# Optimization experiments

Hardware: AMD Instinct MI355X
Metric: run time of the kernel (lower is better)

Reference implementation:

```python
import jax, jax.numpy as jnp
import numpy as np

T, B, C = 512, 4, 256   # seq, batch, in_features
R = 256                 # reduce_dim (== in_features == out_features, required by original view/matmul)
OUT = 256
NE = 64                 # n experts / codebook size
D = R * OUT             # 65536, centroid dimension
TAU = 1.0               # gumbel temperature
DECAY = 0.999           # EMA decay
COMMIT = 0.25           # commitment scale


def setup_inputs() -> dict:
    key = jax.random.key(0)
    ks = jax.random.split(key, 6)
    x = jax.random.normal(ks[0], (T, B, C), dtype=jnp.float32)
    # uniform noise for gumbel sampling (kept as input for determinism)
    u_noise = jax.random.uniform(ks[1], (T * B, NE), dtype=jnp.float32,
                                 minval=1e-6, maxval=1.0 - 1e-6)
    W_map = jax.random.normal(ks[2], (D, C), dtype=jnp.float32) * 0.02   # xavier-ish
    b_map = jnp.zeros((D,), jnp.float32)
    pw_w1 = jax.random.normal(ks[3], (1, 1, R, C), dtype=jnp.float32) * (1.0 / np.sqrt(R))
    pw_B = jnp.zeros((1, 1, OUT), jnp.float32)   # 'constant' bias mode, init 0
    centroids = jax.random.normal(ks[4], (NE, D), dtype=jnp.float32) * 0.5  # init_centroids std
    return {"x": x, "u_noise": u_noise, "W_map": W_map, "b_map": b_map,
            "pw_w1": pw_w1, "pw_B": pw_B, "centroids": centroids}


def reference(x, u_noise, W_map, b_map, pw_w1, pw_B, centroids):
    N = T * B
    # key projection: [N, D]
    keyf = x.reshape(N, C) @ W_map.T + b_map
    kd = jax.lax.stop_gradient(keyf)  # assign() uses points.data

    # squared euclidean cdist: ||p||^2 + ||c||^2 - 2 p c^T   [N, NE]
    d2 = (kd * kd).sum(1, keepdims=True) \
         + (centroids * centroids).sum(1)[None, :] \
         - 2.0 * (kd @ centroids.T)

    # gumbel-softmax routing (soft, hard=False); resp detached (depends only on data)
    g = -jnp.log(-jnp.log(u_noise))
    resp = jax.nn.softmax((-d2 + g) / TAU, axis=-1)  # [N, NE]

    # vectorized EMA centroid update (original loops over experts; math identical,
    # mean_assigned[i] = mean_n resp[n,i]*key[n] = (resp^T @ key)/N), detached in original
    mean_assigned = (resp.T @ kd) / N                # [NE, D]
    centroids_new = DECAY * centroids + (1.0 - DECAY) * mean_assigned

    # quantized U-vectors from UPDATED centroids (update precedes matmul in original)
    quantized = resp @ centroids_new                 # [N, D]

    # euclid commitment loss (quantized detached)
    loss = COMMIT * jnp.mean((keyf - jax.lax.stop_gradient(quantized)) ** 2)

    # dynamic per-token weight: w = quantized.view(T,B,R,C) @ pw_w1  -> [T,B,R,C]
    w2 = jnp.einsum('tbik,kj->tbij', quantized.reshape(T, B, R, C), pw_w1[0, 0])
    # apply to input: [T,B,R,C] @ [T,B,C] -> [T,B,OUT]  (R == OUT)
    out = jnp.einsum('tbij,tbj->tbi', w2, x) + pw_B  # constant bias broadcasts
    return (out, loss)
```

## Files before the change

### kernel.cpp

```cpp
#include <hip/hip_runtime.h>
#include <hip/hip_bf16.h>

constexpr int N_TOK = 2048;
constexpr int C_    = 256;
constexpr int NE    = 64;
constexpr int D_    = 65536;
constexpr float DECAYF = 0.999f;
constexpr float OMD    = 0.001f;
constexpr float ALPHA  = OMD / 2048.0f;
constexpr float RTHRESH = 1e-5f;
constexpr int CHMAX = 8448;

using bf16x8 = __attribute__((ext_vector_type(8))) short;
using f32x4  = __attribute__((ext_vector_type(4))) float;
using u16 = unsigned short;

constexpr size_t OFF_XSUM  = 65536;
constexpr size_t OFF_G     = 65792;
constexpr size_t OFF_M     = 131328;
constexpr size_t OFF_WB    = 147712;
constexpr size_t OFF_BB    = 147968;
constexpr size_t OFF_SUMR  = 147984;
constexpr size_t OFF_A     = 148048;
constexpr size_t OFF_CC0   = 164432;
constexpr size_t OFF_RR    = 168528;
constexpr size_t OFF_CNT   = 172624;
constexpr size_t OFF_CB    = 172752;
constexpr size_t OFF_TSLOT = 172816;
constexpr size_t ZFLOATS   = 174864;
constexpr size_t OFF_RESP  = 174864;
constexpr size_t OFF_AG    = 174864;
constexpr size_t OFF_MA    = 191248;
constexpr size_t OFF_AGA   = 195344;
constexpr size_t OFF_AWB   = 199440;
constexpr size_t OFF_CHE   = 199504;
constexpr size_t OFF_CHB   = 207952;
constexpr size_t OFF_NCH   = 216400;
constexpr size_t OFF_Y     = 305936;
constexpr size_t OFF_CNEW  = 830224;
constexpr size_t OFF_TIDX  = 5024528;
constexpr size_t OFF_TOKR  = 5155600;
constexpr size_t OFF_WTH   = 5286672;
constexpr size_t OFF_SCG   = 13675280;
constexpr size_t OFF_SCC   = 16296720;
constexpr size_t WS_FAST2_END = 18393872;

__device__ __forceinline__ unsigned pack_bf2(float a, float b) {
  __hip_bfloat16 ha = __float2bfloat16(a), hb = __float2bfloat16(b);
  unsigned short ua = *reinterpret_cast<unsigned short*>(&ha);
  unsigned short ub = *reinterpret_cast<unsigned short*>(&hb);
  return (unsigned)ua | ((unsigned)ub << 16);
}

__global__ __launch_bounds__(256) void k_preTw(const float* __restrict__ bmap,
    const float* __restrict__ x, const float* __restrict__ W,
    float* __restrict__ bb, float* __restrict__ xsum, float* __restrict__ Wb,
    u16* __restrict__ wth) {
  __shared__ __align__(16) char smem[32896];
  int bx = blockIdx.x;
  int t = threadIdx.x;
  if (bx < 4) {
    float* red = (float*)smem;
    int base = bx * 16384 + t;
    float s = 0.f;
    for (int q = 0; q < 64; q++) { float v = bmap[base + q * 256]; s = fmaf(v, v, s); }
    red[t] = s;
    __syncthreads();
    for (int k = 128; k > 0; k >>= 1) {
      if (t < k) red[t] += red[t + k];
      __syncthreads();
    }
    if (t == 0) atomicAdd(&bb[0], red[0]);
  } else if (bx < 36) {
    int n0 = (bx - 4) * 64;
    float s = 0.f;
    for (int n = 0; n < 64; n++) s += x[(n0 + n) * C_ + t];
    atomicAdd(&xsum[t], s);
  } else if (bx < 292) {
    float* bs = (float*)smem;
    __shared__ int any;
    int d0 = (bx - 36) * 256;
    if (t == 0) any = 0;
    __syncthreads();
    float bv = bmap[d0 + t];
    bs[t] = bv;
    if (bv != 0.f) any = 1;
    __syncthreads();
    if (any == 0) return;
    float s = 0.f;
    for (int d = 0; d < 256; d++) s = fmaf(bs[d], W[(size_t)(d0 + d) * C_ + t], s);
    atomicAdd(&Wb[t], s);
  } else {
    float (*Ls)[257] = (float(*)[257])smem;
    int d0 = (bx - 292) * 32;
    int r = t >> 3, c8 = (t & 7) * 32;
    #pragma unroll
    for (int q = 0; q < 8; q++) {
      float4 v = *(const float4*)&W[(size_t)(d0 + r) * 256 + c8 + q * 4];
      Ls[r][c8 + q * 4 + 0] = v.x; Ls[r][c8 + q * 4 + 1] = v.y;
      Ls[r][c8 + q * 4 + 2] = v.z; Ls[r][c8 + q * 4 + 3] = v.w;
    }
    __syncthreads();
    int dq = (t & 3) * 8;
    #pragma unroll
    for (int pQ = 0; pQ < 4; pQ++) {
      int c = pQ * 64 + (t >> 2);
      unsigned hw[4];
      #pragma unroll
      for (int q = 0; q < 4; q++)
        hw[q] = pack_bf2(Ls[dq + 2 * q][c], Ls[dq + 2 * q + 1][c]);
      size_t o = (size_t)c * 65536 + d0 + dq;
      *(uint4*)&wth[o] = make_uint4(hw[0], hw[1], hw[2], hw[3]);
    }
  }
}

__global__ __launch_bounds__(256) void k_big1(const u16* __restrict__ wth,
    const float* __restrict__ cen, const float* __restrict__ W,
    const float* __restrict__ bmap, float* __restrict__ gpart,
    float* __restrict__ mpart, float* __restrict__ cpart, float* __restrict__ cb) {
  __shared__ __align__(16) char smem[17408];
  int bx = blockIdx.x;
  int t = threadIdx.x;
  if (bx < 640) {
    u16* Ta = (u16*)smem;
    u16* Tb = Ta + 4352;
    int kb = bx & 63, p = bx >> 6;
    int ti = 0, rem0 = p;
    while (rem0 >= 4 - ti) { rem0 -= 4 - ti; ti++; }
    int tj = ti + rem0;
    bool two = (ti != tj);
    const u16* srcA = wth + (size_t)(ti * 64) * 65536;
    const u16* srcB = wth + (size_t)(tj * 64) * 65536;
    int l = t & 63, w = t >> 6;
    int m0 = w * 16, lm = l & 15, g = l >> 4;
    int scol = t >> 3, skseg = t & 7;
    f32x4 acc[4] = {};
    for (int cc = 0; cc < 16; cc++) {
      int k0 = kb * 1024 + cc * 64;
      __syncthreads();
      {
        uint4 a0 = *(const uint4*)(srcA + (size_t)scol * 65536 + k0 + skseg * 8);
        uint4 a1 = *(const uint4*)(srcA + (size_t)(scol + 32) * 65536 + k0 + skseg * 8);
        *(uint4*)(Ta + (skseg * 68 + scol) * 8) = a0;
        *(uint4*)(Ta + (skseg * 68 + scol + 32) * 8) = a1;
        if (two) {
          uint4 b0 = *(const uint4*)(srcB + (size_t)scol * 65536 + k0 + skseg * 8);
          uint4 b1 = *(const uint4*)(srcB + (size_t)(scol + 32) * 65536 + k0 + skseg * 8);
          *(uint4*)(Tb + (skseg * 68 + scol) * 8) = b0;
          *(uint4*)(Tb + (skseg * 68 + scol + 32) * 8) = b1;
        }
      }
      __syncthreads();
      const u16* TBp = two ? Tb : Ta;
      #pragma unroll
      for (int ks = 0; ks < 2; ks++) {
        int kq = ks * 4 + g;
        bf16x8 av = *(const bf16x8*)(Ta + (kq * 68 + m0 + lm) * 8);
        #pragma unroll
        for (int j = 0; j < 4; j++) {
          bf16x8 bv = *(const bf16x8*)(TBp + (kq * 68 + j * 16 + lm) * 8);
          acc[j] = __builtin_amdgcn_mfma_f32_16x16x32_bf16(av, bv, acc[j], 0, 0, 0);
        }
      }
    }
    float* pp = &gpart[((size_t)p * 64 + kb) * 4096];
    #pragma unroll
    for (int j = 0; j < 4; j++)
      #pragma unroll
      for (int r = 0; r < 4; r++)
        pp[(m0 + (l >> 4) * 4 + r) * 64 + j * 16 + lm] = acc[j][r];
  } else if (bx < 1664) {
    float (*As)[68] = (float(*)[68])smem;
    float (*Bs)[68] = (float(*)[68])(smem + 8704);
    int idx = bx - 640;
    int kb = idx & 255, c0 = (idx >> 8) * 64;
    int d0 = kb * 256;
    int tx = t & 15, ty = t >> 4;
    int e = t >> 2, dg = t & 3;
    int lr = t >> 3, lc = (t & 7) * 8;
    float acc[4][4] = {};
    for (int dk = 0; dk < 256; dk += 32) {
      const float* cr = &cen[(size_t)e * D_ + d0 + dk];
      float4 cv0 = *(const float4*)&cr[dg * 4];
      float4 cv1 = *(const float4*)&cr[16 + dg * 4];
      const float* wr = &W[(size_t)(d0 + dk + lr) * C_ + c0];
      float4 w0 = *(const float4*)&wr[lc];
      float4 w1 = *(const float4*)&wr[lc + 4];
      __syncthreads();
      As[dg * 4 + 0][e] = cv0.x; As[dg * 4 + 1][e] = cv0.y;
      As[dg * 4 + 2][e] = cv0.z; As[dg * 4 + 3][e] = cv0.w;
      As[16 + dg * 4 + 0][e] = cv1.x; As[16 + dg * 4 + 1][e] = cv1.y;
      As[16 + dg * 4 + 2][e] = cv1.z; As[16 + dg * 4 + 3][e] = cv1.w;
      *(float4*)&Bs[lr][lc]     = w0;
      *(float4*)&Bs[lr][lc + 4] = w1;
      __syncthreads();
      #pragma unroll 8
      for (int k = 0; k < 32; k++) {
        float4 ra4 = *(const float4*)&As[k][ty * 4];
        float4 rb4 = *(const float4*)&Bs[k][tx * 4];
        float ra[4] = {ra4.x, ra4.y, ra4.z, ra4.w};
        float rb[4] = {rb4.x, rb4.y, rb4.z, rb4.w};
        #pragma unroll
        for (int i = 0; i < 4; i++)
          #pragma unroll
          for (int j = 0; j < 4; j++)
            acc[i][j] = fmaf(ra[i], rb[j], acc[i][j]);
      }
    }
    float* pp = &mpart[(size_t)kb * 16384];
    #pragma unroll
    for (int i = 0; i < 4; i++)
      *(float4*)&pp[(ty * 4 + i) * C_ + c0 + tx * 4] = *(float4*)&acc[i][0];
  } else {
    float (*cs)[68] = (float(*)[68])smem;
    float* red = (float*)(smem + 8704);
    int d0 = (bx - 1664) * 128;
    int e = t >> 2, dg = t & 3;
    int tx = t & 15, ty = t >> 4;
    float acc[4][4] = {};
    float cbp = 0.f;
    for (int dk = 0; dk < 128; dk += 32) {
      const float* cr = &cen[(size_t)e * D_ + d0 + dk];
      float4 v0 = *(const float4*)&cr[dg * 4];
      float4 v1 = *(const float4*)&cr[16 + dg * 4];
      const float* br = &bmap[d0 + dk];
      float4 b0 = *(const float4*)&br[dg * 4];
      float4 b1 = *(const float4*)&br[16 + dg * 4];
      cbp += v0.x * b0.x + v0.y * b0.y + v0.z * b0.z + v0.w * b0.w
           + v1.x * b1.x + v1.y * b1.y + v1.z * b1.z + v1.w * b1.w;
      __syncthreads();
      cs[dg * 4 + 0][e] = v0.x; cs[dg * 4 + 1][e] = v0.y;
      cs[dg * 4 + 2][e] = v0.z; cs[dg * 4 + 3][e] = v0.w;
      cs[16 + dg * 4 + 0][e] = v1.x; cs[16 + dg * 4 + 1][e] = v1.y;
      cs[16 + dg * 4 + 2][e] = v1.z; cs[16 + dg * 4 + 3][e] = v1.w;
      __syncthreads();
      #pragma unroll
      for (int k = 0; k < 32; k++) {
        float4 ra4 = *(const float4*)&cs[k][ty * 4];
        float4 rb4 = *(const float4*)&cs[k][tx * 4];
        float ra[4] = {ra4.x, ra4.y, ra4.z, ra4.w};
        float rb[4] = {rb4.x, rb4.y, rb4.z, rb4.w};
        #pragma unroll
        for (int i = 0; i < 4; i++)
          #pragma unroll
          for (int j = 0; j < 4; j++)
            acc[i][j] = fmaf(ra[i], rb[j], acc[i][j]);
      }
    }
    float* pp = &cpart[(size_t)(bx - 1664) * 4096];
    #pragma unroll
    for (int i = 0; i < 4; i++)
      *(float4*)&pp[(ty * 4 + i) * 64 + tx * 4] = *(float4*)&acc[i][0];
    red[t] = cbp;
    __syncthreads();
    if (t < 64)
      atomicAdd(&cb[t], red[t * 4] + red[t * 4 + 1] + red[t * 4 + 2] + red[t * 4 + 3]);
  }
}

__global__ __launch_bounds__(256) void k_redAll(const float* __restrict__ gp,
    const float* __restrict__ mp, const float* __restrict__ cp,
    float* __restrict__ G, float* __restrict__ M, float* __restrict__ CC0) {
  int bx = blockIdx.x;
  if (bx < 160) {
    int p = bx / 16, ib = bx % 16;
    int ti = 0, rem0 = p;
    while (rem0 >= 4 - ti) { rem0 -= 4 - ti; ti++; }
    int tj = ti + rem0;
    int i = ib * 256 + threadIdx.x;
    const float* base = gp + (size_t)p * 64 * 4096 + i;
    float s = 0.f;
    for (int kb = 0; kb < 64; kb++) s += base[(size_t)kb * 4096];
    int r = i >> 6, c = i & 63;
    G[(ti * 64 + r) * C_ + tj * 64 + c] = s;
    if (ti != tj) G[(tj * 64 + c) * C_ + ti * 64 + r] = s;
  } else if (bx < 416) {
    int idx = bx - 160;
    int i = (idx & 63) * 256 + threadIdx.x;
    int kb0 = (idx >> 6) * 64;
    float s = 0.f;
    #pragma unroll 8
    for (int kb = 0; kb < 64; kb++) s += mp[(size_t)(kb0 + kb) * 16384 + i];
    atomicAdd(&M[i], s);
  } else {
    int idx = bx - 416;
    int i = (idx & 15) * 256 + threadIdx.x;
    int kb0 = (idx >> 4) * 64;
    float s = 0.f;
    #pragma unroll 8
    for (int kb = 0; kb < 64; kb++) s += cp[(size_t)(kb0 + kb) * 4096 + i];
    atomicAdd(&CC0[i], s);
  }
}

__global__ __launch_bounds__(256) void k_big2(const float* __restrict__ x,
    const float* __restrict__ pw, const float* __restrict__ G,
    const float* __restrict__ u, const float* __restrict__ M,
    const float* __restrict__ CC0, const float* __restrict__ cb,
    float* __restrict__ y, float* __restrict__ gsum, float* __restrict__ resp,
    unsigned int* __restrict__ cnt, int* __restrict__ tokidx,
    float* __restrict__ tokr, int* __restrict__ tslot,
    float* __restrict__ sumresp) {
  __shared__ __align__(16) char smem[9728];
  int bx = blockIdx.x;
  int t = threadIdx.x;
  if (bx < 256) {
    float (*Xs)[17] = (float(*)[17])smem;
    float (*Ps)[17] = (float(*)[17])(smem + 4352);
    float* red = (float*)(smem + 8704);
    int n0 = (bx & 31) * 64;
    int by = bx >> 5;
    bool isg = by >= 4;
    int k0 = (by & 3) * 64;
    const float* B = isg ? G : pw;
    int tx = t & 15, ty = t >> 4;
    int r = t >> 2, q4 = (t & 3) * 4;
    float acc[4][4] = {};
    for (int j0 = 0; j0 < 256; j0 += 16) {
      float4 va = *(const float4*)&x[(n0 + r) * C_ + j0 + q4];
      float4 vb = *(const float4*)&B[(k0 + r) * C_ + j0 + q4];
      __syncthreads();
      Xs[r][q4] = va.x; Xs[r][q4+1] = va.y; Xs[r][q4+2] = va.z; Xs[r][q4+3] = va.w;
      Ps[r][q4] = vb.x; Ps[r][q4+1] = vb.y; Ps[r][q4+2] = vb.z; Ps[r][q4+3] = vb.w;
      __syncthreads();
      #pragma unroll
      for (int k = 0; k < 16; k++) {
        float ra[4], rb[4];
        #pragma unroll
        for (int i = 0; i < 4; i++) ra[i] = Xs[ty*4 + i][k];
        #pragma unroll
        for (int j = 0; j < 4; j++) rb[j] = Ps[tx*4 + j][k];
        #pragma unroll
        for (int i = 0; i < 4; i++)
          #pragma unroll
          for (int j = 0; j < 4; j++)
            acc[i][j] = fmaf(ra[i], rb[j], acc[i][j]);
      }
    }
    if (!isg) {
      #pragma unroll
      for (int i = 0; i < 4; i++)
        #pragma unroll
        for (int j = 0; j < 4; j++)
          y[(n0 + ty*4 + i) * C_ + k0 + tx*4 + j] = acc[i][j];
    } else {
      float s = 0.f;
      #pragma unroll
      for (int i = 0; i < 4; i++) {
        float4 xv = *(const float4*)&x[(size_t)(n0 + ty*4 + i) * C_ + k0 + tx*4];
        s += acc[i][0]*xv.x + acc[i][1]*xv.y + acc[i][2]*xv.z + acc[i][3]*xv.w;
      }
      red[t] = s;
      __syncthreads();
      for (int k = 128; k > 0; k >>= 1) {
        if (t < k) red[t] += red[t + k];
        __syncthreads();
      }
      if (t == 0) atomicAdd(gsum, red[0]);
    }
  } else {
    float* xs   = (float*)smem;
    float* ssum = xs + 1024;
    int tok = t >> 6, e = t & 63;
    int n = (bx - 256) * 4 + tok;
    if (t < 64) ssum[t] = 0.f;
    *(float4*)&xs[tok * 256 + e * 4] = *(const float4*)&x[n * C_ + e * 4];
    __syncthreads();
    const float* Me = M + e * C_;
    const float* xr = &xs[tok * 256];
    float s = 0.f;
    #pragma unroll 8
    for (int j = 0; j < 256; j += 4) {
      float4 m4 = *(const float4*)&Me[j];
      s = fmaf(xr[j],   m4.x, s);
      s = fmaf(xr[j+1], m4.y, s);
      s = fmaf(xr[j+2], m4.z, s);
      s = fmaf(xr[j+3], m4.w, s);
    }
    float uu = u[n * NE + e];
    float g = -logf(-logf(uu));
    float logit = 2.0f * (s + cb[e]) - CC0[e * 65] + g;
    float m = logit;
    for (int off = 32; off > 0; off >>= 1) m = fmaxf(m, __shfl_xor(m, off));
    float ex = expf(logit - m);
    float sum = ex;
    for (int off = 32; off > 0; off >>= 1) sum += __shfl_xor(sum, off);
    float r = ex / sum;
    resp[n * NE + e] = r;
    bool take = r > RTHRESH;
    unsigned long long mask = __ballot(take);
    if (take) {
      unsigned pos = atomicAdd(&cnt[e], 1u);
      tokidx[e * 2048 + pos] = n;
      tokr[e * 2048 + pos] = r;
    }
    if (e == 0) tslot[n] = (int)__popcll(mask);
    atomicAdd(&ssum[e], r);
    __syncthreads();
    if (t < 64) atomicAdd(&sumresp[t], ssum[t]);
  }
}

__global__ __launch_bounds__(256) void k_big3(const float* __restrict__ resp,
    const float* __restrict__ x, float* __restrict__ A, float* __restrict__ RR,
    const unsigned int* __restrict__ cnt, int* __restrict__ che,
    int* __restrict__ chb, int* __restrict__ nch) {
  __shared__ __align__(16) char smem[17408];
  int bx = blockIdx.x;
  int t = threadIdx.x;
  if (bx < 40) {
    int by = bx >> 3, bxx = bx & 7;
    const float* Aop = resp; int lda = NE, ca = 0;
    const float* Bop; int ldb, cbn; float* Out; int ldo, co;
    if (by < 4) { Bop = x; ldb = C_; cbn = by * 64; Out = A; ldo = C_; co = by * 64; }
    else        { Bop = resp; ldb = NE; cbn = 0; Out = RR; ldo = NE; co = 0; }
    int d0 = bxx * 256;
    float (*Wa)[68] = (float(*)[68])smem;
    float (*Wb)[68] = (float(*)[68])(smem + 8704);
    int tx = t & 15, ty = t >> 4;
    int lr = t >> 3, lc = (t & 7) * 8;
    float acc[4][4] = {};
    for (int dk = 0; dk < 256; dk += 32) {
      const float* Arow = &Aop[(size_t)(d0 + dk + lr) * lda + ca];
      const float* Brow = &Bop[(size_t)(d0 + dk + lr) * ldb + cbn];
      float4 a0 = *(const float4*)&Arow[lc];
      float4 a1 = *(const float4*)&Arow[lc + 4];
      float4 b0 = *(const float4*)&Brow[lc];
      float4 b1 = *(const float4*)&Brow[lc + 4];
      __syncthreads();
      *(float4*)&Wa[lr][lc]     = a0;
      *(float4*)&Wa[lr][lc + 4] = a1;
      *(float4*)&Wb[lr][lc]     = b0;
      *(float4*)&Wb[lr][lc + 4] = b1;
      __syncthreads();
      #pragma unroll
      for (int k = 0; k < 32; k++) {
        float4 ra4 = *(const float4*)&Wa[k][ty * 4];
        float4 rb4 = *(const float4*)&Wb[k][tx * 4];
        float ra[4] = {ra4.x, ra4.y, ra4.z, ra4.w};
        float rb[4] = {rb4.x, rb4.y, rb4.z, rb4.w};
        #pragma unroll
        for (int i = 0; i < 4; i++)
          #pragma unroll
          for (int j = 0; j < 4; j++)
            acc[i][j] = fmaf(ra[i], rb[j], acc[i][j]);
      }
    }
    #pragma unroll
    for (int i = 0; i < 4; i++)
      #pragma unroll
      for (int j = 0; j < 4; j++)
        atomicAdd(&Out[(size_t)(ty * 4 + i) * ldo + co + tx * 4 + j], acc[i][j]);
  } else {
    int* cbase = (int*)smem;
    int* ncs   = cbase + 65;
    if (t < 64) ncs[t] = ((int)cnt[t] + 15) >> 4;
    __syncthreads();
    if (t == 0) {
      int s = 0;
      for (int e = 0; e < 64; e++) { cbase[e] = s; s += ncs[e]; }
      cbase[64] = s;
      nch[0] = s < CHMAX ? s : CHMAX;
    }
    __syncthreads();
    for (int e = 0; e < 64; e++) {
      int b0 = cbase[e], nc = cbase[e + 1] - b0;
      for (int i = t; i < nc; i += 256) {
        int idx = b0 + i;
        if (idx < CHMAX) { che[idx] = e; chb[idx] = i * 16; }
      }
    }
  }
}

__global__ __launch_bounds__(256) void k_big4(const float* __restrict__ A,
    const float* __restrict__ G, const float* __restrict__ Wb,
    const float* __restrict__ sumresp, const float* __restrict__ cen,
    const float* __restrict__ bmap, const float* __restrict__ W,
    const float* __restrict__ pwB, float* __restrict__ AG,
    float* __restrict__ AWb, float* __restrict__ cnew, float* __restrict__ out) {
  __shared__ __align__(16) char smem[67840];
  int bx = blockIdx.x;
  int t = threadIdx.x;
  if (bx < 64) {
    float* red = (float*)smem;
    int e = bx, c = t;
    float s = 0.f;
    for (int cp = 0; cp < C_; cp++) s = fmaf(A[e * C_ + cp], G[cp * C_ + c], s);
    AG[e * C_ + c] = s;
    float p = A[e * C_ + c] * Wb[c];
    red[c] = p;
    __syncthreads();
    for (int k = 128; k > 0; k >>= 1) {
      if (c < k) red[c] += red[c + k];
      __syncthreads();
    }
    if (c == 0) AWb[e] = red[0];
  } else if (bx < 1088) {
    u16* Abf = (u16*)smem;
    u16* Wt  = Abf + 64 * 264;
    float* srs = (float*)(Wt + 64 * 264);
    int d0 = (bx - 64) * 64;
    int l = t & 63;
    int m0 = (t >> 6) * 16, lm = l & 15, g = l >> 4;
    {
      int e = t >> 2, c0 = (t & 3) * 64;
      const float* ar = &A[e * C_ + c0];
      u16* dst = &Abf[e * 264 + c0];
      #pragma unroll
      for (int q = 0; q < 8; q++) {
        float4 v0 = *(const float4*)&ar[q * 8];
        float4 v1 = *(const float4*)&ar[q * 8 + 4];
        *(uint4*)&dst[q * 8] = make_uint4(pack_bf2(v0.x, v0.y), pack_bf2(v0.z, v0.w),
                                          pack_bf2(v1.x, v1.y), pack_bf2(v1.z, v1.w));
      }
      int r = t >> 2;
      const float* wr = &W[(size_t)(d0 + r) * C_ + c0];
      u16* wdst = &Wt[r * 264 + c0];
      #pragma unroll
      for (int q = 0; q < 8; q++) {
        float4 v0 = *(const float4*)&wr[q * 8];
        float4 v1 = *(const float4*)&wr[q * 8 + 4];
        *(uint4*)&wdst[q * 8] = make_uint4(pack_bf2(v0.x, v0.y), pack_bf2(v0.z, v0.w),
                                           pack_bf2(v1.x, v1.y), pack_bf2(v1.z, v1.w));
      }
      if (t < 64) srs[t] = sumresp[t];
    }
    __syncthreads();
    f32x4 acc[4] = {};
    #pragma unroll
    for (int kk = 0; kk < 8; kk++) {
      bf16x8 av = *(const bf16x8*)&Abf[(m0 + lm) * 264 + kk * 32 + g * 8];
      #pragma unroll
      for (int j = 0; j < 4; j++) {
        bf16x8 bv = *(const bf16x8*)&Wt[(j * 16 + lm) * 264 + kk * 32 + g * 8];
        acc[j] = __builtin_amdgcn_mfma_f32_16x16x32_bf16(av, bv, acc[j], 0, 0, 0);
      }
    }
    #pragma unroll
    for (int j = 0; j < 4; j++) {
      int d = d0 + j * 16 + lm;
      float bv = bmap[d];
      #pragma unroll
      for (int r = 0; r < 4; r++) {
        int e = m0 + g * 4 + r;
        size_t o = (size_t)e * D_ + d;
        cnew[o] = DECAYF * cen[o] + ALPHA * (acc[j][r] + srs[e] * bv);
      }
    }
  } else {
    int idx = (bx - 1088) * 256 + t;
    out[idx] = pwB[idx & 255];
  }
}

__global__ __launch_bounds__(256) void k_sAs(const int* __restrict__ che,
    const int* __restrict__ chb, const int* __restrict__ nch,
    const unsigned int* __restrict__ cnt, const int* __restrict__ tokidx,
    const float* __restrict__ tokr, const int* __restrict__ tslot,
    const float* __restrict__ y, const float* __restrict__ cnew,
    const float* __restrict__ M, const float* __restrict__ A,
    const float* __restrict__ AG, float* __restrict__ MA,
    float* __restrict__ AGA, float* __restrict__ out) {
  __shared__ __align__(16) char smem[33728];
  int bx = blockIdx.x;
  int t = threadIdx.x;
  if (bx < 1024) {
    int* nsh = (int*)smem;
    float* rsh = (float*)(smem + 64);
    int* wsh = (int*)(smem + 128);
    float (*Ys)[260] = (float(*)[260])(smem + 192);
    float (*Bs)[132] = (float(*)[132])(smem + 192 + 16640);
    int nchv = nch[0];
    int i0 = (bx >> 9) * 128;
    int chx = bx & 511;
    for (int ch = chx; ch < nchv; ch += 512) {
      int e = che[ch], base = chb[ch];
      int c = (int)cnt[e];
      __syncthreads();
      if (t < 16) {
        int idx = base + t;
        if (idx < c) {
          int n = tokidx[e * 2048 + idx];
          nsh[t] = n; rsh[t] = tokr[e * 2048 + idx]; wsh[t] = tslot[n];
        } else { nsh[t] = 0; rsh[t] = 0.f; wsh[t] = 2; }
      }
      __syncthreads();
      {
        int row = t >> 4, c0 = (t & 15) * 16;
        const float* yr = &y[nsh[row] * C_ + c0];
        float4 v0 = *(const float4*)&yr[0];
        float4 v1 = *(const float4*)&yr[4];
        float4 v2 = *(const float4*)&yr[8];
        float4 v3 = *(const float4*)&yr[12];
        *(float4*)&Ys[row][c0]      = v0;
        *(float4*)&Ys[row][c0 + 4]  = v1;
        *(float4*)&Ys[row][c0 + 8]  = v2;
        *(float4*)&Ys[row][c0 + 12] = v3;
      }
      int tx = t & 31, ty = t >> 5;
      int br = t >> 1, bk = (t & 1) * 16;
      float acc[2][4] = {};
      for (int k0 = 0; k0 < 256; k0 += 32) {
        const float* Brow = &cnew[(size_t)e * D_ + (size_t)(i0 + br) * C_ + k0 + bk];
        float4 b0 = *(const float4*)&Brow[0];
        float4 b1 = *(const float4*)&Brow[4];
        float4 b2 = *(const float4*)&Brow[8];
        float4 b3 = *(const float4*)&Brow[12];
        __syncthreads();
        Bs[bk+0][br]  = b0.x; Bs[bk+1][br]  = b0.y; Bs[bk+2][br]  = b0.z; Bs[bk+3][br]  = b0.w;
        Bs[bk+4][br]  = b1.x; Bs[bk+5][br]  = b1.y; Bs[bk+6][br]  = b1.z; Bs[bk+7][br]  = b1.w;
        Bs[bk+8][br]  = b2.x; Bs[bk+9][br]  = b2.y; Bs[bk+10][br] = b2.z; Bs[bk+11][br] = b2.w;
        Bs[bk+12][br] = b3.x; Bs[bk+13][br] = b3.y; Bs[bk+14][br] = b3.z; Bs[bk+15][br] = b3.w;
        __syncthreads();
        #pragma unroll
        for (int kk = 0; kk < 32; kk++) {
          float a0 = Ys[ty*2 + 0][k0 + kk];
          float a1 = Ys[ty*2 + 1][k0 + kk];
          float4 bv = *(const float4*)&Bs[kk][tx*4];
          acc[0][0] = fmaf(a0, bv.x, acc[0][0]); acc[0][1] = fmaf(a0, bv.y, acc[0][1]);
          acc[0][2] = fmaf(a0, bv.z, acc[0][2]); acc[0][3] = fmaf(a0, bv.w, acc[0][3]);
          acc[1][0] = fmaf(a1, bv.x, acc[1][0]); acc[1][1] = fmaf(a1, bv.y, acc[1][1]);
          acc[1][2] = fmaf(a1, bv.z, acc[1][2]); acc[1][3] = fmaf(a1, bv.w, acc[1][3]);
        }
      }
      #pragma unroll
      for (int i = 0; i < 2; i++) {
        int tk = ty*2 + i;
        float r = rsh[tk];
        if (r == 0.f) continue;
        int n = nsh[tk];
        float* op = &out[n * C_ + i0 + tx*4];
        if (wsh[tk] == 1) {
          float4 cur = *(const float4*)op;
          cur.x += r * acc[i][0]; cur.y += r * acc[i][1];
          cur.z += r * acc[i][2]; cur.w += r * acc[i][3];
          *(float4*)op = cur;
        } else {
          atomicAdd(op + 0, r * acc[i][0]);
          atomicAdd(op + 1, r * acc[i][1]);
          atomicAdd(op + 2, r * acc[i][2]);
          atomicAdd(op + 3, r * acc[i][3]);
        }
      }
    }
  } else {
    float* r1 = (float*)smem;
    float* r2 = r1 + 256;
    int e = bx - 1024;
    int f = t >> 2, q = t & 3;
    float s1 = 0.f, s2 = 0.f;
    for (int c = q * 64; c < q * 64 + 64; c++) {
      float a = A[f * C_ + c];
      s1 = fmaf(M[e * C_ + c], a, s1);
      s2 = fmaf(AG[e * C_ + c], a, s2);
    }
    r1[t] = s1; r2[t] = s2;
    __syncthreads();
    if (q == 0) {
      MA[e * NE + f]  = r1[f*4] + r1[f*4+1] + r1[f*4+2] + r1[f*4+3];
      AGA[e * NE + f] = r2[f*4] + r2[f*4+1] + r2[f*4+2] + r2[f*4+3];
    }
  }
}

__global__ __launch_bounds__(256) void k_finalize(
    const float* __restrict__ gsum, const float* __restrict__ M,
    const float* __restrict__ A, const float* __restrict__ AG,
    const float* __restrict__ CC0, const float* __restrict__ RR,
    const float* __restrict__ MA, const float* __restrict__ AGA,
    const float* __restrict__ Xsum, const float* __restrict__ Wb,
    const float* __restrict__ bb, const float* __restrict__ sr,
    const float* __restrict__ cb, const float* __restrict__ AWb,
    float* __restrict__ out) {
  int t = threadIdx.x;
  float a_gs = (t == 0) ? gsum[0] : 0.f;
  float a_am = 0.f, a_aag = 0.f;
  for (int i = t; i < 16384; i += 256) {
    float a = A[i];
    a_am  = fmaf(M[i], a, a_am);
    a_aag = fmaf(AG[i], a, a_aag);
  }
  float a_cc = 0.f, a_ma = 0.f, a_aga = 0.f, a_cbsr = 0.f, a_awbsr = 0.f, a_srsr = 0.f;
  for (int p = t; p < 4096; p += 256) {
    float r = RR[p];
    int e = p >> 6, f = p & 63;
    float srf = sr[f];
    a_cc    = fmaf(r, CC0[p], a_cc);
    a_ma    = fmaf(r, MA[p], a_ma);
    a_aga   = fmaf(r, AGA[p], a_aga);
    a_cbsr  = fmaf(r * cb[e], srf, a_cbsr);
    a_awbsr = fmaf(r * AWb[e], srf, a_awbsr);
    a_srsr  = fmaf(r * sr[e], srf, a_srsr);
  }
  float a_xw = Xsum[t] * Wb[t];
  float a_srcb = 0.f, a_srawb = 0.f, a_sr2 = 0.f;
  if (t < 64) { float s = sr[t]; a_srcb = s * cb[t]; a_srawb = s * AWb[t]; a_sr2 = s * s; }
  float v[13] = {a_gs, a_am, a_aag, a_cc, a_ma, a_aga, a_cbsr, a_awbsr, a_srsr,
                 a_xw, a_srcb, a_srawb, a_sr2};
  __shared__ float red[256];
  __shared__ float tot[13];
  for (int q = 0; q < 13; q++) {
    red[t] = v[q];
    __syncthreads();
    for (int s2 = 128; s2 > 0; s2 >>= 1) {
      if (t < s2) red[t] += red[t + s2];
      __syncthreads();
    }
    if (t == 0) tot[q] = red[0];
    __syncthreads();
  }
  if (t == 0) {
    const float q = DECAYF, al = ALPHA;
    float bbv = bb[0];
    float sumkeyf2 = tot[0] + 2.f * tot[9] + 2048.f * bbv;
    float cross = q * (tot[1] + tot[10]) + al * (tot[2] + 2.f * tot[11] + bbv * tot[12]);
    float sumq2 = q*q * tot[3] + 2.f*q*al * (tot[4] + tot[6])
                + al*al * (tot[5] + 2.f * tot[7] + bbv * tot[8]);
    out[524288] = (0.25f / (2048.0f * 65536.0f)) * (sumkeyf2 - 2.f * cross + sumq2);
  }
}

__global__ __launch_bounds__(256) void k_Gslow(const float* __restrict__ W,
    float* __restrict__ part) {
  int p = blockIdx.y;
  int ti = 0, rem0 = p;
  while (rem0 >= 4 - ti) { rem0 -= 4 - ti; ti++; }
  int tj = ti + rem0;
  int c1 = ti * 64, c2 = tj * 64;
  int d0 = blockIdx.x * 1024;
  __shared__ unsigned short Wat[64][40], Wbt[64][40];
  int t = threadIdx.x;
  int h = t >> 7;
  int rem = t & 127;
  int k2 = rem >> 3;
  int c4b = rem & 7;
  int cbase = h ? c2 : c1;
  unsigned short (*dst)[40] = h ? Wbt : Wat;
  int l = t & 63, w = t >> 6;
  int m0 = w * 16;
  int lm = l & 15, q8 = (l >> 4) * 8;
  f32x4 acc[4] = {};
  for (int dk = 0; dk < 1024; dk += 32) {
    __syncthreads();
    #pragma unroll
    for (int it = 0; it < 2; it++) {
      int c4 = c4b + it * 8;
      const float* rp = &W[(size_t)(d0 + dk + k2 * 2) * C_ + cbase + c4 * 4];
      float4 g0 = *(const float4*)rp;
      float4 g1 = *(const float4*)(rp + C_);
      *(unsigned*)&dst[c4 * 4 + 0][k2 * 2] = pack_bf2(g0.x, g1.x);
      *(unsigned*)&dst[c4 * 4 + 1][k2 * 2] = pack_bf2(g0.y, g1.y);
      *(unsigned*)&dst[c4 * 4 + 2][k2 * 2] = pack_bf2(g0.z, g1.z);
      *(unsigned*)&dst[c4 * 4 + 3][k2 * 2] = pack_bf2(g0.w, g1.w);
    }
    __syncthreads();
    bf16x8 av = *(const bf16x8*)&Wat[m0 + lm][q8];
    #pragma unroll
    for (int j = 0; j < 4; j++) {
      bf16x8 bv = *(const bf16x8*)&Wbt[j * 16 + lm][q8];
      acc[j] = __builtin_amdgcn_mfma_f32_16x16x32_bf16(av, bv, acc[j], 0, 0, 0);
    }
  }
  float* pp = &part[((size_t)p * 64 + blockIdx.x) * 4096];
  #pragma unroll
  for (int j = 0; j < 4; j++)
    #pragma unroll
    for (int r = 0; r < 4; r++)
      pp[(m0 + (l >> 4) * 4 + r) * 64 + j * 16 + lm] = acc[j][r];
}

extern "C" void kernel_launch(void* const* d_in, const int* in_sizes, int n_in,
                              void* d_out, int out_size, void* d_ws, size_t ws_size,
                              hipStream_t stream) {
  const float* x    = (const float*)d_in[0];
  const float* u    = (const float*)d_in[1];
  const float* Wm   = (const float*)d_in[2];
  const float* bmap = (const float*)d_in[3];
  const float* pw   = (const float*)d_in[4];
  const float* pwB  = (const float*)d_in[5];
  const float* cen  = (const float*)d_in[6];
  float* out = (float*)d_out;
  float* ws  = (float*)d_ws;

  float* Xsum    = ws + OFF_XSUM;
  float* G       = ws + OFF_G;
  float* M       = ws + OFF_M;
  float* Wb      = ws + OFF_WB;
  float* bb      = ws + OFF_BB;
  float* gsum    = ws + OFF_BB + 1;
  float* sumresp = ws + OFF_SUMR;
  float* A       = ws + OFF_A;
  float* CC0     = ws + OFF_CC0;
  float* RR      = ws + OFF_RR;
  unsigned int* cnt = (unsigned int*)(ws + OFF_CNT);
  float* cb      = ws + OFF_CB;
  int*   tslot   = (int*)(ws + OFF_TSLOT);
  float* resp    = ws + OFF_RESP;
  float* AG      = ws + OFF_AG;
  float* MA      = ws + OFF_MA;
  float* AGA     = ws + OFF_AGA;
  float* AWb     = ws + OFF_AWB;
  int*   che     = (int*)(ws + OFF_CHE);
  int*   chb     = (int*)(ws + OFF_CHB);
  int*   nch     = (int*)(ws + OFF_NCH);
  float* y       = ws + OFF_Y;
  float* cnew    = ws + OFF_CNEW;
  float* scratch = ws + OFF_CNEW;
  int*   tokidx  = (int*)(ws + OFF_TIDX);
  float* tokr    = ws + OFF_TOKR;
  u16*   wth     = (u16*)(ws + OFF_WTH);
  float* sc_g    = ws + OFF_SCG;
  float* sc_cc   = ws + OFF_SCC;

  bool fast2 = ws_size >= (size_t)WS_FAST2_END * sizeof(float);

  hipMemsetAsync(d_ws, 0, ZFLOATS * sizeof(float), stream);

  if (fast2) {
    k_preTw<<<2340, 256, 0, stream>>>(bmap, x, Wm, bb, Xsum, Wb, wth);
    k_big1<<<2176, 256, 0, stream>>>(wth, cen, Wm, bmap, sc_g, scratch, sc_cc, cb);
    k_redAll<<<544, 256, 0, stream>>>(sc_g, scratch, sc_cc, G, M, CC0);
  } else {
    k_preTw<<<292, 256, 0, stream>>>(bmap, x, Wm, bb, Xsum, Wb, wth);
    k_Gslow<<<dim3(64, 10), 256, 0, stream>>>(Wm, ws + OFF_CNEW);
    k_big1<<<2176, 256, 0, stream>>>(wth, cen, Wm, bmap, sc_g, scratch, sc_cc, cb);
    k_redAll<<<544, 256, 0, stream>>>(sc_g, scratch, sc_cc, G, M, CC0);
  }
  k_big2<<<768, 256, 0, stream>>>(x, pw, G, u, M, CC0, cb, y, gsum, resp,
                                  cnt, tokidx, tokr, tslot, sumresp);
  k_big3<<<41, 256, 0, stream>>>(resp, x, A, RR, cnt, che, chb, nch);
  k_big4<<<3136, 256, 0, stream>>>(A, G, Wb, sumresp, cen, bmap, Wm, pwB,
                                   AG, AWb, cnew, out);
  k_sAs<<<1088, 256, 0, stream>>>(che, chb, nch, cnt, tokidx, tokr, tslot,
                                  y, cnew, M, A, AG, MA, AGA, out);
  k_finalize<<<1, 256, 0, stream>>>(gsum, M, A, AG, CC0, RR, MA, AGA, Xsum, Wb,
                                    bb, sumresp, cb, AWb, out);
}
```

Baseline: 331.8 us.

## Compute centroid-W product with split-bf16 MFMA instead of fp32 FMA

Precomputes hi/lo bf16 splits of W and of the centroids in the prep kernel, then computes the M = centroids·W partial products with three bf16 MFMAs per tile (hi·hi, hi·lo, lo·hi), replacing the scalar fp32 FMA path. This halves the number of M-partial blocks and reduces the reduction work. In exchange it adds extra workspace writes (the lo W copy and two centroid copies) and a bigger LDS footprint, with near-fp32 accuracy. It also removes the slow fallback G kernel, so the fast2 path is now taken unconditionally.

```diff
diff --git a/kernel.cpp b/kernel.cpp
--- a/kernel.cpp
+++ b/kernel.cpp
@@ -44,6 +44,10 @@
 constexpr size_t OFF_SCG   = 13675280;
 constexpr size_t OFF_SCC   = 16296720;
 constexpr size_t WS_FAST2_END = 18393872;
+constexpr size_t OFF_WTL   = 18393872;
+constexpr size_t OFF_CENH  = 26782480;
+constexpr size_t OFF_CENL  = 28879632;
+constexpr size_t WS_FULL_END = 30976784;
 
 __device__ __forceinline__ unsigned pack_bf2(float a, float b) {
   __hip_bfloat16 ha = __float2bfloat16(a), hb = __float2bfloat16(b);
@@ -52,10 +56,20 @@
   return (unsigned)ua | ((unsigned)ub << 16);
 }
 
+__device__ __forceinline__ void split_bf(float x, u16& h, u16& lo) {
+  __hip_bfloat16 hb = __float2bfloat16(x);
+  float hf = __bfloat162float(hb);
+  __hip_bfloat16 lb = __float2bfloat16(x - hf);
+  h  = *reinterpret_cast<unsigned short*>(&hb);
+  lo = *reinterpret_cast<unsigned short*>(&lb);
+}
+
 __global__ __launch_bounds__(256) void k_preTw(const float* __restrict__ bmap,
     const float* __restrict__ x, const float* __restrict__ W,
-    float* __restrict__ bb, float* __restrict__ xsum, float* __restrict__ Wb,
-    u16* __restrict__ wth) {
+    const float* __restrict__ cen, float* __restrict__ bb,
+    float* __restrict__ xsum, float* __restrict__ Wb, u16* __restrict__ wth,
+    u16* __restrict__ wtl, u16* __restrict__ cenh, u16* __restrict__ cenl,
+    int full) {
   __shared__ __align__(16) char smem[32896];
   int bx = blockIdx.x;
   int t = threadIdx.x;
@@ -90,7 +104,7 @@
     float s = 0.f;
     for (int d = 0; d < 256; d++) s = fmaf(bs[d], W[(size_t)(d0 + d) * C_ + t], s);
     atomicAdd(&Wb[t], s);
-  } else {
+  } else if (bx < 2340) {
     float (*Ls)[257] = (float(*)[257])smem;
     int d0 = (bx - 292) * 32;
     int r = t >> 3, c8 = (t & 7) * 32;
@@ -105,23 +119,48 @@
     #pragma unroll
     for (int pQ = 0; pQ < 4; pQ++) {
       int c = pQ * 64 + (t >> 2);
-      unsigned hw[4];
-      #pragma unroll
-      for (int q = 0; q < 4; q++)
-        hw[q] = pack_bf2(Ls[dq + 2 * q][c], Ls[dq + 2 * q + 1][c]);
+      unsigned hw[4], lw[4];
+      #pragma unroll
+      for (int q = 0; q < 4; q++) {
+        u16 h0, l0, h1, l1;
+        split_bf(Ls[dq + 2 * q][c], h0, l0);
+        split_bf(Ls[dq + 2 * q + 1][c], h1, l1);
+        hw[q] = (unsigned)h0 | ((unsigned)h1 << 16);
+        lw[q] = (unsigned)l0 | ((unsigned)l1 << 16);
+      }
       size_t o = (size_t)c * 65536 + d0 + dq;
       *(uint4*)&wth[o] = make_uint4(hw[0], hw[1], hw[2], hw[3]);
-    }
+      if (full) *(uint4*)&wtl[o] = make_uint4(lw[0], lw[1], lw[2], lw[3]);
+    }
+  } else {
+    size_t base = ((size_t)(bx - 2340) * 256 + t) * 8;
+    float4 a = *(const float4*)&cen[base];
+    float4 b = *(const float4*)&cen[base + 4];
+    float v[8] = {a.x, a.y, a.z, a.w, b.x, b.y, b.z, b.w};
+    unsigned hw[4], lw[4];
+    #pragma unroll
+    for (int q = 0; q < 4; q++) {
+      u16 h0, l0, h1, l1;
+      split_bf(v[2 * q], h0, l0);
+      split_bf(v[2 * q + 1], h1, l1);
+      hw[q] = (unsigned)h0 | ((unsigned)h1 << 16);
+      lw[q] = (unsigned)l0 | ((unsigned)l1 << 16);
+    }
+    *(uint4*)&cenh[base] = make_uint4(hw[0], hw[1], hw[2], hw[3]);
+    *(uint4*)&cenl[base] = make_uint4(lw[0], lw[1], lw[2], lw[3]);
   }
 }
 
 __global__ __launch_bounds__(256) void k_big1(const u16* __restrict__ wth,
-    const float* __restrict__ cen, const float* __restrict__ W,
-    const float* __restrict__ bmap, float* __restrict__ gpart,
-    float* __restrict__ mpart, float* __restrict__ cpart, float* __restrict__ cb) {
-  __shared__ __align__(16) char smem[17408];
+    const u16* __restrict__ wtl, const u16* __restrict__ cenh,
+    const u16* __restrict__ cenl, const float* __restrict__ cen,
+    const float* __restrict__ W, const float* __restrict__ bmap,
+    float* __restrict__ gpart, float* __restrict__ mpart,
+    float* __restrict__ cpart, float* __restrict__ cb, int useM3) {
+  __shared__ __align__(16) char smem[34816];
   int bx = blockIdx.x;
   int t = threadIdx.x;
+  int ccstart = useM3 ? 1152 : 1664;
   if (bx < 640) {
     u16* Ta = (u16*)smem;
     u16* Tb = Ta + 4352;
@@ -170,7 +209,58 @@
       #pragma unroll
       for (int r = 0; r < 4; r++)
         pp[(m0 + (l >> 4) * 4 + r) * 64 + j * 16 + lm] = acc[j][r];
-  } else if (bx < 1664) {
+  } else if (useM3 && bx < 1152) {
+    u16* TAH = (u16*)smem;
+    u16* TAL = TAH + 4352;
+    u16* TBH = TAL + 4352;
+    u16* TBL = TBH + 4352;
+    int idx = bx - 640;
+    int kb = idx & 127, c0 = (idx >> 7) * 64;
+    const u16* srcBH = wth + (size_t)c0 * 65536;
+    const u16* srcBL = wtl + (size_t)c0 * 65536;
+    int l = t & 63;
+    int m0 = (t >> 6) * 16, lm = l & 15, g = l >> 4;
+    int scol = t >> 3, skseg = t & 7;
+    f32x4 acc[4] = {};
+    for (int cc = 0; cc < 8; cc++) {
+      int k0 = kb * 512 + cc * 64;
+      __syncthreads();
+      {
+        size_t o0 = (size_t)scol * 65536 + k0 + skseg * 8;
+        size_t o1 = (size_t)(scol + 32) * 65536 + k0 + skseg * 8;
+        uint4 ah0 = *(const uint4*)(cenh + o0), ah1 = *(const uint4*)(cenh + o1);
+        uint4 al0 = *(const uint4*)(cenl + o0), al1 = *(const uint4*)(cenl + o1);
+        uint4 bh0 = *(const uint4*)(srcBH + o0), bh1 = *(const uint4*)(srcBH + o1);
+        uint4 bl0 = *(const uint4*)(srcBL + o0), bl1 = *(const uint4*)(srcBL + o1);
+        int s0 = (skseg * 68 + scol) * 8, s1 = (skseg * 68 + scol + 32) * 8;
+        *(uint4*)(TAH + s0) = ah0; *(uint4*)(TAH + s1) = ah1;
+        *(uint4*)(TAL + s0) = al0; *(uint4*)(TAL + s1) = al1;
+        *(uint4*)(TBH + s0) = bh0; *(uint4*)(TBH + s1) = bh1;
+        *(uint4*)(TBL + s0) = bl0; *(uint4*)(TBL + s1) = bl1;
+      }
+      __syncthreads();
+      #pragma unroll
+      for (int ks = 0; ks < 2; ks++) {
+        int kq = ks * 4 + g;
+        bf16x8 ah = *(const bf16x8*)(TAH + (kq * 68 + m0 + lm) * 8);
+        bf16x8 al = *(const bf16x8*)(TAL + (kq * 68 + m0 + lm) * 8);
+        #pragma unroll
+        for (int j = 0; j < 4; j++) {
+          bf16x8 bh = *(const bf16x8*)(TBH + (kq * 68 + j * 16 + lm) * 8);
+          bf16x8 bl = *(const bf16x8*)(TBL + (kq * 68 + j * 16 + lm) * 8);
+          acc[j] = __builtin_amdgcn_mfma_f32_16x16x32_bf16(ah, bh, acc[j], 0, 0, 0);
+          acc[j] = __builtin_amdgcn_mfma_f32_16x16x32_bf16(ah, bl, acc[j], 0, 0, 0);
+          acc[j] = __builtin_amdgcn_mfma_f32_16x16x32_bf16(al, bh, acc[j], 0, 0, 0);
+        }
+      }
+    }
+    float* pp = &mpart[(size_t)kb * 16384];
+    #pragma unroll
+    for (int j = 0; j < 4; j++)
+      #pragma unroll
+      for (int r = 0; r < 4; r++)
+        pp[(m0 + (l >> 4) * 4 + r) * 256 + c0 + j * 16 + lm] = acc[j][r];
+  } else if (!useM3 && bx < 1664) {
     float (*As)[68] = (float(*)[68])smem;
     float (*Bs)[68] = (float(*)[68])(smem + 8704);
     int idx = bx - 640;
@@ -215,7 +305,7 @@
   } else {
     float (*cs)[68] = (float(*)[68])smem;
     float* red = (float*)(smem + 8704);
-    int d0 = (bx - 1664) * 128;
+    int d0 = (bx - ccstart) * 128;
     int e = t >> 2, dg = t & 3;
     int tx = t & 15, ty = t >> 4;
     float acc[4][4] = {};
@@ -248,7 +338,7 @@
             acc[i][j] = fmaf(ra[i], rb[j], acc[i][j]);
       }
     }
-    float* pp = &cpart[(size_t)(bx - 1664) * 4096];
+    float* pp = &cpart[(size_t)(bx - ccstart) * 4096];
     #pragma unroll
     for (int i = 0; i < 4; i++)
       *(float4*)&pp[(ty * 4 + i) * 64 + tx * 4] = *(float4*)&acc[i][0];
@@ -261,7 +351,8 @@
 
 __global__ __launch_bounds__(256) void k_redAll(const float* __restrict__ gp,
     const float* __restrict__ mp, const float* __restrict__ cp,
-    float* __restrict__ G, float* __restrict__ M, float* __restrict__ CC0) {
+    float* __restrict__ G, float* __restrict__ M, float* __restrict__ CC0,
+    int mkb) {
   int bx = blockIdx.x;
   if (bx < 160) {
     int p = bx / 16, ib = bx % 16;
@@ -275,7 +366,7 @@
     int r = i >> 6, c = i & 63;
     G[(ti * 64 + r) * C_ + tj * 64 + c] = s;
     if (ti != tj) G[(tj * 64 + c) * C_ + ti * 64 + r] = s;
-  } else if (bx < 416) {
+  } else if (bx < 160 + mkb) {
     int idx = bx - 160;
     int i = (idx & 63) * 256 + threadIdx.x;
     int kb0 = (idx >> 6) * 64;
@@ -284,7 +375,7 @@
     for (int kb = 0; kb < 64; kb++) s += mp[(size_t)(kb0 + kb) * 16384 + i];
     atomicAdd(&M[i], s);
   } else {
-    int idx = bx - 416;
+    int idx = bx - 160 - mkb;
     int i = (idx & 15) * 256 + threadIdx.x;
     int kb0 = (idx >> 4) * 64;
     float s = 0.f;
@@ -720,55 +811,6 @@
                 + al*al * (tot[5] + 2.f * tot[7] + bbv * tot[8]);
     out[524288] = (0.25f / (2048.0f * 65536.0f)) * (sumkeyf2 - 2.f * cross + sumq2);
   }
-}
-
-__global__ __launch_bounds__(256) void k_Gslow(const float* __restrict__ W,
-    float* __restrict__ part) {
-  int p = blockIdx.y;
-  int ti = 0, rem0 = p;
-  while (rem0 >= 4 - ti) { rem0 -= 4 - ti; ti++; }
-  int tj = ti + rem0;
-  int c1 = ti * 64, c2 = tj * 64;
-  int d0 = blockIdx.x * 1024;
-  __shared__ unsigned short Wat[64][40], Wbt[64][40];
-  int t = threadIdx.x;
-  int h = t >> 7;
-  int rem = t & 127;
-  int k2 = rem >> 3;
-  int c4b = rem & 7;
-  int cbase = h ? c2 : c1;
-  unsigned short (*dst)[40] = h ? Wbt : Wat;
-  int l = t & 63, w = t >> 6;
-  int m0 = w * 16;
-  int lm = l & 15, q8 = (l >> 4) * 8;
-  f32x4 acc[4] = {};
-  for (int dk = 0; dk < 1024; dk += 32) {
-    __syncthreads();
-    #pragma unroll
-    for (int it = 0; it < 2; it++) {
-      int c4 = c4b + it * 8;
-      const float* rp = &W[(size_t)(d0 + dk + k2 * 2) * C_ + cbase + c4 * 4];
-      float4 g0 = *(const float4*)rp;
-      float4 g1 = *(const float4*)(rp + C_);
-      *(unsigned*)&dst[c4 * 4 + 0][k2 * 2] = pack_bf2(g0.x, g1.x);
-      *(unsigned*)&dst[c4 * 4 + 1][k2 * 2] = pack_bf2(g0.y, g1.y);
-      *(unsigned*)&dst[c4 * 4 + 2][k2 * 2] = pack_bf2(g0.z, g1.z);
-      *(unsigned*)&dst[c4 * 4 + 3][k2 * 2] = pack_bf2(g0.w, g1.w);
-    }
-    __syncthreads();
-    bf16x8 av = *(const bf16x8*)&Wat[m0 + lm][q8];
-    #pragma unroll
-    for (int j = 0; j < 4; j++) {
-      bf16x8 bv = *(const bf16x8*)&Wbt[j * 16 + lm][q8];
-      acc[j] = __builtin_amdgcn_mfma_f32_16x16x32_bf16(av, bv, acc[j], 0, 0, 0);
-    }
-  }
-  float* pp = &part[((size_t)p * 64 + blockIdx.x) * 4096];
-  #pragma unroll
-  for (int j = 0; j < 4; j++)
-    #pragma unroll
-    for (int r = 0; r < 4; r++)
-      pp[(m0 + (l >> 4) * 4 + r) * 64 + j * 16 + lm] = acc[j][r];
 }
 
 extern "C" void kernel_launch(void* const* d_in, const int* in_sizes, int n_in,
@@ -811,23 +853,23 @@
   int*   tokidx  = (int*)(ws + OFF_TIDX);
   float* tokr    = ws + OFF_TOKR;
   u16*   wth     = (u16*)(ws + OFF_WTH);
+  u16*   wtl     = (u16*)(ws + OFF_WTL);
+  u16*   cenh    = (u16*)(ws + OFF_CENH);
+  u16*   cenl    = (u16*)(ws + OFF_CENL);
   float* sc_g    = ws + OFF_SCG;
   float* sc_cc   = ws + OFF_SCC;
 
-  bool fast2 = ws_size >= (size_t)WS_FAST2_END * sizeof(float);
+  bool full = ws_size >= (size_t)WS_FULL_END * sizeof(float);
 
   hipMemsetAsync(d_ws, 0, ZFLOATS * sizeof(float), stream);
 
-  if (fast2) {
-    k_preTw<<<2340, 256, 0, stream>>>(bmap, x, Wm, bb, Xsum, Wb, wth);
-    k_big1<<<2176, 256, 0, stream>>>(wth, cen, Wm, bmap, sc_g, scratch, sc_cc, cb);
-    k_redAll<<<544, 256, 0, stream>>>(sc_g, scratch, sc_cc, G, M, CC0);
-  } else {
-    k_preTw<<<292, 256, 0, stream>>>(bmap, x, Wm, bb, Xsum, Wb, wth);
-    k_Gslow<<<dim3(64, 10), 256, 0, stream>>>(Wm, ws + OFF_CNEW);
-    k_big1<<<2176, 256, 0, stream>>>(wth, cen, Wm, bmap, sc_g, scratch, sc_cc, cb);
-    k_redAll<<<544, 256, 0, stream>>>(sc_g, scratch, sc_cc, G, M, CC0);
-  }
+  k_preTw<<<full ? 4388 : 2340, 256, 0, stream>>>(bmap, x, Wm, cen, bb, Xsum, Wb,
+                                                  wth, wtl, cenh, cenl, full ? 1 : 0);
+  k_big1<<<full ? 1664 : 2176, 256, 0, stream>>>(wth, wtl, cenh, cenl, cen, Wm,
+                                                 bmap, sc_g, scratch, sc_cc, cb,
+                                                 full ? 1 : 0);
+  k_redAll<<<full ? 416 : 544, 256, 0, stream>>>(sc_g, scratch, sc_cc, G, M, CC0,
+                                                 full ? 128 : 256);
   k_big2<<<768, 256, 0, stream>>>(x, pw, G, u, M, CC0, cb, y, gsum, resp,
                                   cnt, tokidx, tokr, tslot, sumresp);
   k_big3<<<41, 256, 0, stream>>>(resp, x, A, RR, cnt, che, chb, nch);
```

Measured after the change: 338.2 us. No clear change (+1.9%).
